# Kernel optimization log

Measured on AMD Instinct MI355X. Metric: run time of the kernel, lower is better.

Reference implementation:

```python
import jax, jax.numpy as jnp
import numpy as np

B, T_TXT, T_IMG, N_LAT = 4, 2048, 8, 64
DIM, DIM_VIS, HEADS, DIM_HEAD = 2048, 1024, 8, 64
INNER = HEADS * DIM_HEAD
LN_EPS = 1e-5


def setup_inputs() -> dict:
    key = jax.random.key(0)
    ks = jax.random.split(key, 8)
    x = jax.random.normal(ks[0], (B, T_TXT, DIM), dtype=jnp.float32)
    media = jax.random.normal(ks[1], (B, T_IMG, N_LAT, DIM_VIS), dtype=jnp.float32)
    # exactly T_IMG media tokens per batch row at random positions
    pos = jax.random.randint(ks[2], (B, T_IMG), 0, T_TXT)
    media_locations = jnp.zeros((B, T_TXT), dtype=bool).at[jnp.arange(B)[:, None], pos].set(True)
    gamma = jnp.ones((DIM,), dtype=jnp.float32)
    beta = jnp.zeros((DIM,), dtype=jnp.float32)
    Wq = jax.random.normal(ks[3], (DIM, INNER), dtype=jnp.float32) * 0.02
    Wkv = jax.random.normal(ks[4], (DIM_VIS, 2 * INNER), dtype=jnp.float32) * 0.02
    Wout = jax.random.normal(ks[5], (INNER, DIM), dtype=jnp.float32) * 0.02
    return {"x": x, "media": media, "media_locations": media_locations,
            "gamma": gamma, "beta": beta, "Wq": Wq, "Wkv": Wkv, "Wout": Wout}


def _split_heads(t, h):
    b, s, _ = t.shape
    return t.reshape(b, s, h, -1).transpose(0, 2, 1, 3)  # b h s d


def reference(x, media, media_locations, gamma, beta, Wq, Wkv, Wout):
    b, t_txt, _ = x.shape
    _, t_img, n, _ = media.shape
    scale = DIM_HEAD ** (-0.5)

    # LayerNorm
    mu = jnp.mean(x, axis=-1, keepdims=True)
    var = jnp.mean(jnp.square(x - mu), axis=-1, keepdims=True)
    xn = (x - mu) * jax.lax.rsqrt(var + LN_EPS) * gamma + beta

    q = _split_heads(xn @ Wq, HEADS) * scale                # b h i d
    media_f = media.reshape(b, t_img * n, -1)               # b (t n) dv
    kv = media_f @ Wkv
    k, v = jnp.split(kv, 2, axis=-1)
    k = _split_heads(k, HEADS)                              # b h j d
    v = _split_heads(v, HEADS)

    sim = jnp.einsum('bhid,bhjd->bhij', q, k)               # b h i (t n)

    text_time = jnp.cumsum(media_locations.astype(jnp.int32), axis=-1)   # b i
    media_time = jnp.repeat(jnp.arange(1, t_img + 1), n)                 # (t n)
    mask = text_time[:, None, :, None] == media_time[None, None, None, :]

    neg = -jnp.finfo(sim.dtype).max
    sim = jnp.where(mask, sim, neg)
    sim = sim - jax.lax.stop_gradient(jnp.max(sim, axis=-1, keepdims=True))
    attn = jax.nn.softmax(sim, axis=-1)
    # zero attention for text tokens that precede any media
    attn = jnp.where((text_time == 0)[:, None, :, None], 0.0, attn)

    out = jnp.einsum('bhij,bhjd->bhid', attn, v)
    out = out.transpose(0, 2, 1, 3).reshape(b, t_txt, INNER)
    return out @ Wout
```

## Files before the change

kernel.cpp:

```cpp
#include <hip/hip_runtime.h>
#include <hip/hip_bf16.h>
#include <stdint.h>

typedef __bf16 bf16_t;
typedef __bf16 bf16x8 __attribute__((ext_vector_type(8)));
typedef float f32x4 __attribute__((ext_vector_type(4)));

#define NB      4
#define T_TXT   2048
#define T_IMG   8
#define N_LAT   64
#define DIM     2048
#define DIM_VIS 1024
#define HEADS   8
#define DHEAD   64
#define INNER   512

__device__ __forceinline__ void gld_lds16(const void* g, void* l) {
    __builtin_amdgcn_global_load_lds((const __attribute__((address_space(1))) void*)g,
                                     (__attribute__((address_space(3))) void*)l,
                                     16, 0, 0);
}

__global__ __launch_bounds__(256) void transpose3_k(const float* __restrict__ Wq,
                                                    const float* __restrict__ Wkv,
                                                    const float* __restrict__ Wout,
                                                    bf16_t* __restrict__ WqT,
                                                    bf16_t* __restrict__ WkvT,
                                                    bf16_t* __restrict__ WoutT) {
    __shared__ float tile[32][33];
    const float* in; bf16_t* out; int R, C;
    int which = blockIdx.y;
    if (which == 0)      { in = Wq;   out = WqT;   R = 2048; C = 512;  }
    else if (which == 1) { in = Wkv;  out = WkvT;  R = 1024; C = 1024; }
    else                 { in = Wout; out = WoutT; R = 512;  C = 2048; }
    int nbx = C >> 5;
    int bx = blockIdx.x % nbx, by = blockIdx.x / nbx;
    int c0 = bx * 32, r0 = by * 32;
    int x = threadIdx.x, y = threadIdx.y;
#pragma unroll
    for (int d = 0; d < 4; d++)
        tile[y + d * 8][x] = in[(size_t)(r0 + y + d * 8) * C + c0 + x];
    __syncthreads();
#pragma unroll
    for (int d = 0; d < 4; d++)
        out[(size_t)(c0 + y + d * 8) * R + r0 + x] = (bf16_t)tile[x][y + d * 8];
}

__global__ __launch_bounds__(256) void cvt_k(const float* __restrict__ in,
                                             bf16_t* __restrict__ out) {
    int idx = (blockIdx.x * 256 + threadIdx.x) * 8;
    f32x4 a = *(const f32x4*)(in + idx);
    f32x4 b = *(const f32x4*)(in + idx + 4);
    bf16x8 o;
#pragma unroll
    for (int i = 0; i < 4; i++) { o[i] = (bf16_t)a[i]; o[i + 4] = (bf16_t)b[i]; }
    *(bf16x8*)(out + idx) = o;
}

__global__ __launch_bounds__(256) void ln_k(const float* __restrict__ x,
                                            const float* __restrict__ gamma,
                                            const float* __restrict__ beta,
                                            bf16_t* __restrict__ xn) {
    int row = blockIdx.x;
    int t = threadIdx.x;
    const float* xp = x + (size_t)row * DIM + t * 8;
    f32x4 v0 = *(const f32x4*)xp;
    f32x4 v1 = *(const f32x4*)(xp + 4);
    float f[8];
    float s = 0.f, ss = 0.f;
#pragma unroll
    for (int i = 0; i < 4; i++) { f[i] = v0[i]; f[i + 4] = v1[i]; }
#pragma unroll
    for (int i = 0; i < 8; i++) { s += f[i]; ss += f[i] * f[i]; }
#pragma unroll
    for (int off = 32; off > 0; off >>= 1) { s += __shfl_xor(s, off); ss += __shfl_xor(ss, off); }
    __shared__ float sbuf[4], sbuf2[4];
    int wid = t >> 6, lane = t & 63;
    if (lane == 0) { sbuf[wid] = s; sbuf2[wid] = ss; }
    __syncthreads();
    s  = sbuf[0] + sbuf[1] + sbuf[2] + sbuf[3];
    ss = sbuf2[0] + sbuf2[1] + sbuf2[2] + sbuf2[3];
    float mu  = s * (1.0f / DIM);
    float var = ss * (1.0f / DIM) - mu * mu;
    float rs  = rsqrtf(var + 1e-5f);
    f32x4 g0 = *(const f32x4*)(gamma + t * 8);
    f32x4 g1 = *(const f32x4*)(gamma + t * 8 + 4);
    f32x4 b0 = *(const f32x4*)(beta + t * 8);
    f32x4 b1 = *(const f32x4*)(beta + t * 8 + 4);
    bf16x8 o;
#pragma unroll
    for (int i = 0; i < 4; i++) {
        o[i]     = (bf16_t)((f[i]     - mu) * rs * g0[i] + b0[i]);
        o[i + 4] = (bf16_t)((f[i + 4] - mu) * rs * g1[i] + b1[i]);
    }
    *(bf16x8*)(xn + (size_t)row * DIM + t * 8) = o;
}

template <int TAG, typename OT>
__global__ __launch_bounds__(256) void gemm_bt(const bf16_t* __restrict__ A,
                                               const bf16_t* __restrict__ Bt,
                                               OT* __restrict__ C,
                                               int M, int N, int K, int Kper,
                                               float scale,
                                               int gx, int gy, int gz) {
    __shared__ __align__(16) bf16_t lA[2][128 * 32];
    __shared__ __align__(16) bf16_t lB[2][128 * 32];
    int tid = threadIdx.x;
    int w = tid >> 6, lane = tid & 63;
    int wm = w >> 1, wn = w & 1;

    int nwg = gx * gy * gz;
    int cpx = nwg >> 3;
    int nid = (blockIdx.x & 7) * cpx + (blockIdx.x >> 3);
    int tpy = gx * gz;
    int by = nid / tpy;
    int rr = nid - by * tpy;
    int bz = rr / gx;
    int bx = rr - bz * gx;

    int bm0 = by * 128, bn0 = bx * 128;
    int kbase = bz * Kper;
    int q = lane >> 4, l16 = lane & 15;

    int c0 = w * 64 + lane;
    int r0 = c0 >> 2, cc0 = c0 & 3;
    int c1 = 256 + c0;
    int r1 = c1 >> 2, cc1 = c1 & 3;
    const bf16_t* pA0 = A + (size_t)(bm0 + r0) * K + kbase + cc0 * 8;
    const bf16_t* pA1 = A + (size_t)(bm0 + r1) * K + kbase + cc1 * 8;
    const bf16_t* pB0 = Bt + (size_t)(bn0 + r0) * K + kbase + cc0 * 8;
    const bf16_t* pB1 = Bt + (size_t)(bn0 + r1) * K + kbase + cc1 * 8;

    f32x4 acc[4][4];
#pragma unroll
    for (int i = 0; i < 4; i++)
#pragma unroll
        for (int j = 0; j < 4; j++)
            acc[i][j] = (f32x4){0.f, 0.f, 0.f, 0.f};

    auto stage = [&](int buf, int k0) {
        gld_lds16(pA0 + k0, &lA[buf][w * 512]);
        gld_lds16(pA1 + k0, &lA[buf][2048 + w * 512]);
        gld_lds16(pB0 + k0, &lB[buf][w * 512]);
        gld_lds16(pB1 + k0, &lB[buf][2048 + w * 512]);
    };
    auto compute = [&](int buf) {
        bf16x8 af[4], bfr[4];
#pragma unroll
        for (int mt = 0; mt < 4; mt++)
            af[mt] = *(const bf16x8*)(&lA[buf][(wm * 64 + mt * 16 + l16) * 32 + q * 8]);
#pragma unroll
        for (int nt = 0; nt < 4; nt++)
            bfr[nt] = *(const bf16x8*)(&lB[buf][(wn * 64 + nt * 16 + l16) * 32 + q * 8]);
#pragma unroll
        for (int mt = 0; mt < 4; mt++)
#pragma unroll
            for (int nt = 0; nt < 4; nt++)
                acc[mt][nt] = __builtin_amdgcn_mfma_f32_16x16x32_bf16(af[mt], bfr[nt], acc[mt][nt], 0, 0, 0);
    };

    stage(0, 0);
    __syncthreads();
    int cur = 0;
    for (int k0 = 32; k0 < Kper; k0 += 32) {
        stage(cur ^ 1, k0);
        compute(cur);
        __syncthreads();
        cur ^= 1;
    }
    compute(cur);

    OT* Cz = C + (size_t)bz * M * N;
#pragma unroll
    for (int mt = 0; mt < 4; mt++)
#pragma unroll
        for (int nt = 0; nt < 4; nt++)
#pragma unroll
            for (int r = 0; r < 4; r++) {
                int row = bm0 + wm * 64 + mt * 16 + q * 4 + r;
                int col = bn0 + wn * 64 + nt * 16 + l16;
                Cz[(size_t)row * N + col] = (OT)(acc[mt][nt][r] * scale);
            }
}

__global__ __launch_bounds__(256) void reduce4_k(const bf16_t* __restrict__ p,
                                                 bf16_t* __restrict__ o,
                                                 size_t n, float scale) {
    size_t i = ((size_t)blockIdx.x * 256 + threadIdx.x) * 8;
    bf16x8 a0 = *(const bf16x8*)(p + i);
    bf16x8 a1 = *(const bf16x8*)(p + n + i);
    bf16x8 a2 = *(const bf16x8*)(p + 2 * n + i);
    bf16x8 a3 = *(const bf16x8*)(p + 3 * n + i);
    bf16x8 r;
#pragma unroll
    for (int u = 0; u < 8; u++)
        r[u] = (bf16_t)(((float)a0[u] + (float)a1[u] + (float)a2[u] + (float)a3[u]) * scale);
    *(bf16x8*)(o + i) = r;
}

__global__ __launch_bounds__(256) void cumsum_bucket_k(const void* __restrict__ locs,
                                                       int* __restrict__ bstart,
                                                       int* __restrict__ bcnt) {
    int b = blockIdx.x, t = threadIdx.x;
    const unsigned* up = (const unsigned*)locs;
    const int* ip = (const int*)locs;
    const unsigned char* bp = (const unsigned char*)locs;
    const float* fp = (const float*)locs;

    int other = 0, nf = 0;
#pragma unroll
    for (int i = 0; i < 8; i++) {
        unsigned wv = up[t * 8 + i];
        nf    += (wv == 0x3F800000u);
        other += (wv != 0u && wv != 1u && wv != 0x3F800000u);
    }
#pragma unroll
    for (int off = 32; off > 0; off >>= 1) { other += __shfl_xor(other, off); nf += __shfl_xor(nf, off); }
    __shared__ int so[4], sf[4];
    int wid = t >> 6, lane = t & 63;
    if (lane == 0) { so[wid] = other; sf[wid] = nf; }
    __syncthreads();
    other = so[0] + so[1] + so[2] + so[3];
    nf    = sf[0] + sf[1] + sf[2] + sf[3];
    int mode = (other > 0) ? 0 : ((nf > 0) ? 2 : 1);

    int v[8];
    int s = 0;
#pragma unroll
    for (int i = 0; i < 8; i++) {
        int idx = b * T_TXT + t * 8 + i;
        int xv;
        if (mode == 1)      xv = ip[idx];
        else if (mode == 0) xv = (int)bp[idx];
        else                xv = (fp[idx] != 0.f) ? 1 : 0;
        v[i] = xv;
        s += xv;
    }
    __shared__ int sc[256];
    __shared__ int sstart[T_IMG];
    if (t < T_IMG) sstart[t] = T_TXT;
    sc[t] = s;
    __syncthreads();
    for (int off = 1; off < 256; off <<= 1) {
        int add = (t >= off) ? sc[t - off] : 0;
        __syncthreads();
        sc[t] += add;
        __syncthreads();
    }
    int run = sc[t] - s;
#pragma unroll
    for (int i = 0; i < 8; i++) {
        run += v[i];
        if (v[i] && run <= T_IMG) sstart[run - 1] = t * 8 + i;
    }
    __syncthreads();
    if (t < T_IMG) {
        int st = sstart[t];
        int nx = (t + 1 < T_IMG) ? sstart[t + 1] : T_TXT;
        bstart[b * T_IMG + t] = st;
        bcnt[b * T_IMG + t]   = nx - st;
    }
}

__global__ __launch_bounds__(256) void attn_mfma_k(const bf16_t* __restrict__ q,
                                                   const bf16_t* __restrict__ kv,
                                                   const int* __restrict__ bstart,
                                                   const int* __restrict__ bcnt,
                                                   bf16_t* __restrict__ aout) {
    __shared__ __align__(16) bf16_t lK[64 * 64];
    __shared__ __align__(16) bf16_t lVt[64 * 64];
    __shared__ __align__(16) bf16_t lP[4][16 * 64];

    int bucket = blockIdx.x >> 3;
    int h = blockIdx.x & 7;
    int n_q = bcnt[bucket];
    if (n_q <= 0) return;
    int b = bucket >> 3;
    int timg = bucket & 7;
    int row0 = b * T_TXT + bstart[bucket];
    size_t krow0 = (size_t)(b * (T_IMG * N_LAT) + timg * N_LAT);

    int tid = threadIdx.x;
    int wid = tid >> 6, lane = tid & 63;
    int quad = lane >> 4, l16 = lane & 15;

    {
        const bf16_t* s0 = kv + (krow0 + 16 * wid + (lane >> 3)) * (2 * INNER) + h * DHEAD + (lane & 7) * 8;
        const bf16_t* s1 = kv + (krow0 + 16 * wid + 8 + (lane >> 3)) * (2 * INNER) + h * DHEAD + (lane & 7) * 8;
        gld_lds16(s0, lK + wid * 1024);
        gld_lds16(s1, lK + wid * 1024 + 512);
    }
    {
        int key = tid & 63, dblk = tid >> 6;
        const bf16_t* vsrc = kv + (krow0 + key) * (2 * INNER) + INNER + h * DHEAD + dblk * 16;
        bf16x8 v0 = *(const bf16x8*)vsrc;
        bf16x8 v1 = *(const bf16x8*)(vsrc + 8);
#pragma unroll
        for (int u = 0; u < 8; u++) {
            lVt[(dblk * 16 + u) * 64 + key]     = v0[u];
            lVt[(dblk * 16 + 8 + u) * 64 + key] = v1[u];
        }
    }
    __syncthreads();

    for (int c0 = wid * 16; c0 < n_q; c0 += 64) {
        int qi = row0 + c0 + ((c0 + l16 < n_q) ? l16 : 0);

        const bf16_t* qrow = q + (size_t)qi * INNER + h * DHEAD + quad * 8;
        bf16x8 qf0 = *(const bf16x8*)qrow;
        bf16x8 qf1 = *(const bf16x8*)(qrow + 32);
        f32x4 s[4];
#pragma unroll
        for (int nt = 0; nt < 4; nt++) s[nt] = (f32x4){0.f, 0.f, 0.f, 0.f};
#pragma unroll
        for (int nt = 0; nt < 4; nt++) {
            bf16x8 kf0 = *(const bf16x8*)(lK + (l16 + 16 * nt) * 64 + quad * 8);
            bf16x8 kf1 = *(const bf16x8*)(lK + (l16 + 16 * nt) * 64 + 32 + quad * 8);
            s[nt] = __builtin_amdgcn_mfma_f32_16x16x32_bf16(qf0, kf0, s[nt], 0, 0, 0);
            s[nt] = __builtin_amdgcn_mfma_f32_16x16x32_bf16(qf1, kf1, s[nt], 0, 0, 0);
        }

        float mr[4];
#pragma unroll
        for (int r = 0; r < 4; r++) {
            float m = fmaxf(fmaxf(s[0][r], s[1][r]), fmaxf(s[2][r], s[3][r]));
#pragma unroll
            for (int off = 8; off >= 1; off >>= 1) m = fmaxf(m, __shfl_xor(m, off));
            mr[r] = m;
        }
        float p[4][4];
#pragma unroll
        for (int nt = 0; nt < 4; nt++)
#pragma unroll
            for (int r = 0; r < 4; r++)
                p[nt][r] = __expf(s[nt][r] - mr[r]);
#pragma unroll
        for (int r = 0; r < 4; r++) {
            float tsum = p[0][r] + p[1][r] + p[2][r] + p[3][r];
#pragma unroll
            for (int off = 8; off >= 1; off >>= 1) tsum += __shfl_xor(tsum, off);
            float inv = 1.0f / tsum;
            p[0][r] *= inv; p[1][r] *= inv; p[2][r] *= inv; p[3][r] *= inv;
        }

        bf16_t* pt = lP[wid];
#pragma unroll
        for (int nt = 0; nt < 4; nt++)
#pragma unroll
            for (int r = 0; r < 4; r++)
                pt[(quad * 4 + r) * 64 + 16 * nt + l16] = (bf16_t)p[nt][r];
        asm volatile("s_waitcnt lgkmcnt(0)" ::: "memory");

        bf16x8 pf0 = *(const bf16x8*)(pt + l16 * 64 + quad * 8);
        bf16x8 pf1 = *(const bf16x8*)(pt + l16 * 64 + 32 + quad * 8);
        f32x4 o[4];
#pragma unroll
        for (int ntd = 0; ntd < 4; ntd++) o[ntd] = (f32x4){0.f, 0.f, 0.f, 0.f};
#pragma unroll
        for (int ntd = 0; ntd < 4; ntd++) {
            bf16x8 vf0 = *(const bf16x8*)(lVt + (l16 + 16 * ntd) * 64 + quad * 8);
            bf16x8 vf1 = *(const bf16x8*)(lVt + (l16 + 16 * ntd) * 64 + 32 + quad * 8);
            o[ntd] = __builtin_amdgcn_mfma_f32_16x16x32_bf16(pf0, vf0, o[ntd], 0, 0, 0);
            o[ntd] = __builtin_amdgcn_mfma_f32_16x16x32_bf16(pf1, vf1, o[ntd], 0, 0, 0);
        }

#pragma unroll
        for (int r = 0; r < 4; r++) {
            int qidx = c0 + quad * 4 + r;
            if (qidx < n_q) {
                bf16_t* op = aout + (size_t)(row0 + qidx) * INNER + h * DHEAD + l16;
#pragma unroll
                for (int ntd = 0; ntd < 4; ntd++)
                    op[16 * ntd] = (bf16_t)o[ntd][r];
            }
        }
    }
}

extern "C" void kernel_launch(void* const* d_in, const int* in_sizes, int n_in,
                              void* d_out, int out_size, void* d_ws, size_t ws_size,
                              hipStream_t stream) {
    const float* x     = (const float*)d_in[0];
    const float* media = (const float*)d_in[1];
    const void*  locs  = d_in[2];
    const float* gamma = (const float*)d_in[3];
    const float* beta  = (const float*)d_in[4];
    const float* Wq    = (const float*)d_in[5];
    const float* Wkv   = (const float*)d_in[6];
    const float* Wout  = (const float*)d_in[7];
    float* out = (float*)d_out;

    bf16_t* xn   = (bf16_t*)d_out;
    bf16_t* part = (bf16_t*)d_out + (size_t)16 * 1024 * 1024;

    char* p = (char*)d_ws;
    bf16_t* qbuf   = (bf16_t*)p; p += (size_t)8192 * 512 * 2;
    bf16_t* aout   = (bf16_t*)p; p += (size_t)8192 * 512 * 2;
    bf16_t* kvbuf  = (bf16_t*)p; p += (size_t)2048 * 1024 * 2;
    bf16_t* mediab = (bf16_t*)p; p += (size_t)2048 * 1024 * 2;
    bf16_t* WqT    = (bf16_t*)p; p += (size_t)512 * 2048 * 2;
    bf16_t* WkvT   = (bf16_t*)p; p += (size_t)1024 * 1024 * 2;
    bf16_t* WoutT  = (bf16_t*)p; p += (size_t)2048 * 512 * 2;
    int*    bstart = (int*)p;    p += 32 * sizeof(int);
    int*    bcnt   = (int*)p;    p += 32 * sizeof(int);

    transpose3_k<<<dim3(1024, 3), dim3(32, 8), 0, stream>>>(Wq, Wkv, Wout, WqT, WkvT, WoutT);
    cvt_k<<<(2048 * 1024) / (256 * 8), 256, 0, stream>>>(media, mediab);

    ln_k<<<8192, 256, 0, stream>>>(x, gamma, beta, xn);

    gemm_bt<1, bf16_t><<<1024, 256, 0, stream>>>(xn, WqT, part, 8192, 512, 2048, 512, 1.0f, 4, 64, 4);
    reduce4_k<<<2048, 256, 0, stream>>>(part, qbuf, (size_t)8192 * 512, 0.125f);

    gemm_bt<2, bf16_t><<<512, 256, 0, stream>>>(mediab, WkvT, part, 2048, 1024, 1024, 256, 1.0f, 8, 16, 4);
    reduce4_k<<<1024, 256, 0, stream>>>(part, kvbuf, (size_t)2048 * 1024, 1.0f);

    cumsum_bucket_k<<<NB, 256, 0, stream>>>(locs, bstart, bcnt);

    hipMemsetAsync(aout, 0, (size_t)8192 * 512 * 2, stream);

    attn_mfma_k<<<32 * HEADS, 256, 0, stream>>>(qbuf, kvbuf, bstart, bcnt, aout);

    gemm_bt<3, float><<<1024, 256, 0, stream>>>(aout, WoutT, out, 8192, 2048, 512, 512, 1.0f, 16, 64, 1);
}
```

Measured before the change: 260.5 us.

## Merge Q and KV GEMMs into one launch, drop KV split-K, split attention buckets

Runs the Q projection and the KV projection in a single combined launch. The KV GEMM now does a full-K pass straight into the output buffer, which removes its split-K partial buffer and extra reduce launch. Global-to-LDS loads and the fragment reads are reorganized into a 16-row-per-wave layout, intended to cut LDS bank conflicts. Attention blocks are split into up to 8 chunks of 256 queries per bucket and head, raising occupancy for large buckets at the cost of reloading K/V per chunk and launching many empty blocks.

New measurement: 283.2 us. +8.7%, slower.

```diff
diff --git a/kernel.cpp b/kernel.cpp
--- a/kernel.cpp
+++ b/kernel.cpp
@@ -97,22 +97,21 @@
     *(bf16x8*)(xn + (size_t)row * DIM + t * 8) = o;
 }
 
-template <int TAG, typename OT>
-__global__ __launch_bounds__(256) void gemm_bt(const bf16_t* __restrict__ A,
-                                               const bf16_t* __restrict__ Bt,
-                                               OT* __restrict__ C,
-                                               int M, int N, int K, int Kper,
-                                               float scale,
-                                               int gx, int gy, int gz) {
-    __shared__ __align__(16) bf16_t lA[2][128 * 32];
-    __shared__ __align__(16) bf16_t lB[2][128 * 32];
+template <typename OT>
+__device__ __forceinline__ void gemm_body(const bf16_t* __restrict__ A,
+                                          const bf16_t* __restrict__ Bt,
+                                          OT* __restrict__ C,
+                                          int M, int N, int K, int Kper,
+                                          float scale, int bid,
+                                          int gx, int gy, int gz,
+                                          bf16_t* lA, bf16_t* lB) {
     int tid = threadIdx.x;
     int w = tid >> 6, lane = tid & 63;
     int wm = w >> 1, wn = w & 1;
 
     int nwg = gx * gy * gz;
     int cpx = nwg >> 3;
-    int nid = (blockIdx.x & 7) * cpx + (blockIdx.x >> 3);
+    int nid = (bid & 7) * cpx + (bid >> 3);
     int tpy = gx * gz;
     int by = nid / tpy;
     int rr = nid - by * tpy;
@@ -123,14 +122,11 @@
     int kbase = bz * Kper;
     int q = lane >> 4, l16 = lane & 15;
 
-    int c0 = w * 64 + lane;
-    int r0 = c0 >> 2, cc0 = c0 & 3;
-    int c1 = 256 + c0;
-    int r1 = c1 >> 2, cc1 = c1 & 3;
-    const bf16_t* pA0 = A + (size_t)(bm0 + r0) * K + kbase + cc0 * 8;
-    const bf16_t* pA1 = A + (size_t)(bm0 + r1) * K + kbase + cc1 * 8;
-    const bf16_t* pB0 = Bt + (size_t)(bn0 + r0) * K + kbase + cc0 * 8;
-    const bf16_t* pB1 = Bt + (size_t)(bn0 + r1) * K + kbase + cc1 * 8;
+    int l15 = lane & 15, lq = lane >> 4;
+    const bf16_t* pA0 = A  + (size_t)(bm0 + w * 16      + l15) * K + kbase + lq * 8;
+    const bf16_t* pA1 = A  + (size_t)(bm0 + 64 + w * 16 + l15) * K + kbase + lq * 8;
+    const bf16_t* pB0 = Bt + (size_t)(bn0 + w * 16      + l15) * K + kbase + lq * 8;
+    const bf16_t* pB1 = Bt + (size_t)(bn0 + 64 + w * 16 + l15) * K + kbase + lq * 8;
 
     f32x4 acc[4][4];
 #pragma unroll
@@ -140,19 +136,19 @@
             acc[i][j] = (f32x4){0.f, 0.f, 0.f, 0.f};
 
     auto stage = [&](int buf, int k0) {
-        gld_lds16(pA0 + k0, &lA[buf][w * 512]);
-        gld_lds16(pA1 + k0, &lA[buf][2048 + w * 512]);
-        gld_lds16(pB0 + k0, &lB[buf][w * 512]);
-        gld_lds16(pB1 + k0, &lB[buf][2048 + w * 512]);
+        gld_lds16(pA0 + k0, lA + buf * 4096 + w * 512);
+        gld_lds16(pA1 + k0, lA + buf * 4096 + 2048 + w * 512);
+        gld_lds16(pB0 + k0, lB + buf * 4096 + w * 512);
+        gld_lds16(pB1 + k0, lB + buf * 4096 + 2048 + w * 512);
     };
     auto compute = [&](int buf) {
         bf16x8 af[4], bfr[4];
 #pragma unroll
         for (int mt = 0; mt < 4; mt++)
-            af[mt] = *(const bf16x8*)(&lA[buf][(wm * 64 + mt * 16 + l16) * 32 + q * 8]);
+            af[mt] = *(const bf16x8*)(lA + buf * 4096 + (wm * 4 + mt) * 512 + q * 128 + l16 * 8);
 #pragma unroll
         for (int nt = 0; nt < 4; nt++)
-            bfr[nt] = *(const bf16x8*)(&lB[buf][(wn * 64 + nt * 16 + l16) * 32 + q * 8]);
+            bfr[nt] = *(const bf16x8*)(lB + buf * 4096 + (wn * 4 + nt) * 512 + q * 128 + l16 * 8);
 #pragma unroll
         for (int mt = 0; mt < 4; mt++)
 #pragma unroll
@@ -182,6 +178,29 @@
                 int col = bn0 + wn * 64 + nt * 16 + l16;
                 Cz[(size_t)row * N + col] = (OT)(acc[mt][nt][r] * scale);
             }
+}
+
+__global__ __launch_bounds__(256) void gemm12_k(const bf16_t* __restrict__ xn,
+                                                const bf16_t* __restrict__ WqT,
+                                                bf16_t* __restrict__ part,
+                                                const bf16_t* __restrict__ mediab,
+                                                const bf16_t* __restrict__ WkvT,
+                                                bf16_t* __restrict__ kvbuf) {
+    __shared__ __align__(16) bf16_t lA[2 * 4096];
+    __shared__ __align__(16) bf16_t lB[2 * 4096];
+    int bid = blockIdx.x;
+    if (bid < 1024)
+        gemm_body<bf16_t>(xn, WqT, part, 8192, 512, 2048, 512, 1.0f, bid, 4, 64, 4, lA, lB);
+    else
+        gemm_body<bf16_t>(mediab, WkvT, kvbuf, 2048, 1024, 1024, 1024, 1.0f, bid - 1024, 8, 16, 1, lA, lB);
+}
+
+__global__ __launch_bounds__(256) void gemm3_k(const bf16_t* __restrict__ aout,
+                                               const bf16_t* __restrict__ WoutT,
+                                               float* __restrict__ out) {
+    __shared__ __align__(16) bf16_t lA[2 * 4096];
+    __shared__ __align__(16) bf16_t lB[2 * 4096];
+    gemm_body<float>(aout, WoutT, out, 8192, 2048, 512, 512, 1.0f, blockIdx.x, 16, 64, 1, lA, lB);
 }
 
 __global__ __launch_bounds__(256) void reduce4_k(const bf16_t* __restrict__ p,
@@ -272,10 +291,14 @@
     __shared__ __align__(16) bf16_t lVt[64 * 64];
     __shared__ __align__(16) bf16_t lP[4][16 * 64];
 
-    int bucket = blockIdx.x >> 3;
-    int h = blockIdx.x & 7;
+    int bid = blockIdx.x;
+    int bucket = bid >> 6;
+    int h = (bid >> 3) & 7;
+    int c = bid & 7;
     int n_q = bcnt[bucket];
-    if (n_q <= 0) return;
+    int qlo = c << 8;
+    if (n_q <= qlo) return;
+    int qhi = (n_q < qlo + 256) ? n_q : (qlo + 256);
     int b = bucket >> 3;
     int timg = bucket & 7;
     int row0 = b * T_TXT + bstart[bucket];
@@ -304,7 +327,7 @@
     }
     __syncthreads();
 
-    for (int c0 = wid * 16; c0 < n_q; c0 += 64) {
+    for (int c0 = qlo + wid * 16; c0 < qhi; c0 += 64) {
         int qi = row0 + c0 + ((c0 + l16 < n_q) ? l16 : 0);
 
         const bf16_t* qrow = q + (size_t)qi * INNER + h * DHEAD + quad * 8;
@@ -410,17 +433,14 @@
 
     ln_k<<<8192, 256, 0, stream>>>(x, gamma, beta, xn);
 
-    gemm_bt<1, bf16_t><<<1024, 256, 0, stream>>>(xn, WqT, part, 8192, 512, 2048, 512, 1.0f, 4, 64, 4);
+    gemm12_k<<<1152, 256, 0, stream>>>(xn, WqT, part, mediab, WkvT, kvbuf);
     reduce4_k<<<2048, 256, 0, stream>>>(part, qbuf, (size_t)8192 * 512, 0.125f);
 
-    gemm_bt<2, bf16_t><<<512, 256, 0, stream>>>(mediab, WkvT, part, 2048, 1024, 1024, 256, 1.0f, 8, 16, 4);
-    reduce4_k<<<1024, 256, 0, stream>>>(part, kvbuf, (size_t)2048 * 1024, 1.0f);
-
     cumsum_bucket_k<<<NB, 256, 0, stream>>>(locs, bstart, bcnt);
 
     hipMemsetAsync(aout, 0, (size_t)8192 * 512 * 2, stream);
 
-    attn_mfma_k<<<32 * HEADS, 256, 0, stream>>>(qbuf, kvbuf, bstart, bcnt, aout);
-
-    gemm_bt<3, float><<<1024, 256, 0, stream>>>(aout, WoutT, out, 8192, 2048, 512, 512, 1.0f, 16, 64, 1);
-}
+    attn_mfma_k<<<32 * HEADS * 8, 256, 0, stream>>>(qbuf, kvbuf, bstart, bcnt, aout);
+
+    gemm3_k<<<1024, 256, 0, stream>>>(aout, WoutT, out);
+}
```
